# Kernel optimization log

Hardware: AMD Instinct MI355X
Metric: run time of the kernel (lower is better)

## Reference

```python
import jax, jax.numpy as jnp
import numpy as np

B, T = 64, 1024
RNN_DIM = 256          # lstm input/hidden dim
HID2 = 512             # 2*rnn_hidden_dim (bi-encoder output per char)
POS_DIM = 100
POS_SIZE = 48
LABEL = 96
POS_PAD = 0
APP_ID = 1


def setup_inputs() -> dict:
    key = jax.random.key(0)
    ks = jax.random.split(key, 9)
    s = 0.1
    enc = jax.random.normal(ks[0], (B, T, HID2), jnp.float32)
    pos_id = jax.random.randint(ks[1], (T, B), 0, POS_SIZE)
    start_index = jax.random.randint(ks[2], (T, B), 0, T)
    pos_table = (jax.random.normal(ks[3], (POS_SIZE, POS_DIM), jnp.float32) * s).at[POS_PAD].set(0.0)
    W_ih = jax.random.normal(ks[4], (4 * RNN_DIM, RNN_DIM), jnp.float32) * s
    b_ih = jnp.zeros((4 * RNN_DIM,), jnp.float32)
    W_hh = jax.random.normal(ks[5], (4 * RNN_DIM, RNN_DIM), jnp.float32) * s
    b_hh = jnp.zeros((4 * RNN_DIM,), jnp.float32)
    comb_W = jax.random.normal(ks[6], (RNN_DIM, HID2 + POS_DIM), jnp.float32) * s
    comb_b = jnp.zeros((RNN_DIM,), jnp.float32)
    lin_W = jax.random.normal(ks[7], (LABEL, HID2 + RNN_DIM), jnp.float32) * s
    return {"encoder_out": enc, "pos_table": pos_table, "W_ih": W_ih, "b_ih": b_ih,
            "W_hh": W_hh, "b_hh": b_hh, "comb_W": comb_W, "comb_b": comb_b,
            "lin_W": lin_W, "pos_id": pos_id, "start_index": start_index}


def reference(encoder_out, pos_table, W_ih, b_ih, W_hh, b_hh, comb_W, comb_b, lin_W,
              pos_id, start_index):
    Bn, Tn, D2 = encoder_out.shape
    H = W_hh.shape[1]
    L = lin_W.shape[0]
    dt = encoder_out.dtype
    # prefix sums: P[:, t] = sum of encoder_out[:, :t]  -> [B, T+1, D2]
    P = jnp.concatenate([jnp.zeros((Bn, 1, D2), dt), jnp.cumsum(encoder_out, axis=1)], axis=1)
    # step t consumes decisions made at step t-1 (state.pos_id[-1] / words_startindex[-1])
    prev_pos = jnp.concatenate([jnp.zeros((1, Bn), pos_id.dtype), pos_id[:-1]], axis=0)
    prev_start = jnp.concatenate([jnp.zeros((1, Bn), start_index.dtype), start_index[:-1]], axis=0)
    ts = jnp.arange(Tn)
    enc_t = jnp.swapaxes(encoder_out, 0, 1)   # [T, B, D2]
    P_t = jnp.swapaxes(P[:, :Tn], 0, 1)       # [T, B, D2]; P_t[t] = prefix up to t
    barange = jnp.arange(Bn)
    lab = jnp.arange(L)

    def step(carry, xs):
        h, c = carry
        t, pp, ps, Pt, et = xs
        # variable-length word avg-pool over chars [start, t)  (F.avg_pool1d)
        valid = (ps >= 0) & (t > 0)
        start = jnp.clip(jnp.minimum(ps, t - 1), 0, Tn - 1)
        wsum = Pt - P[barange, start]                       # [B, D2]
        length = jnp.maximum(t - start, 1).astype(dt)
        avg = jnp.where(valid[:, None], wsum / length[:, None], jnp.zeros((), dt))
        pe = pos_table[pp]                                  # [B, pos_dim]
        z = jnp.tanh(jnp.concatenate([pe, avg], axis=1) @ comb_W.T + comb_b)
        z = jnp.where(t > 0, z, jnp.zeros((), dt))          # t==0: z bucket of zeros
        # LSTMCell
        gates = z @ W_ih.T + b_ih + h @ W_hh.T + b_hh
        i_g, f_g, g_g, o_g = jnp.split(gates, 4, axis=1)
        c_new = jax.nn.sigmoid(f_g) * c + jax.nn.sigmoid(i_g) * jnp.tanh(g_g)
        h_new = jax.nn.sigmoid(o_g) * jnp.tanh(c_new)
        # output projection over [h_now, encoder_out[t]]
        out = jnp.concatenate([h_new, et], axis=1) @ lin_W.T
        out = jnp.where((t == 0) & (lab[None, :] == APP_ID), jnp.asarray(-1e10, dt), out)
        return (h_new, c_new), out

    h0 = jnp.zeros((Bn, H), dt)
    (_, _), outs = jax.lax.scan(step, (h0, h0), (ts, prev_pos, prev_start, P_t, enc_t))
    dec = jnp.swapaxes(outs, 0, 1).reshape(Bn * Tn, L)   # cat along dim 1 then view
    return jax.nn.log_softmax(dec, axis=1)
```

## Files before the change

### kernel.cpp

```cpp
#include <hip/hip_runtime.h>

typedef unsigned short u16;
typedef unsigned int u32;
typedef unsigned long long u64;
typedef __attribute__((ext_vector_type(8))) short short8;
typedef __attribute__((ext_vector_type(4))) float f32x4;
typedef __attribute__((ext_vector_type(4))) unsigned int u32x4;

#define B_ 64
#define T_ 1024
#define D2_ 512
#define HD_ 256
#define G4_ 1024
#define PD_ 100
#define KX_ 640
#define KO_ 768
#define LBL_ 96
#define LPAD_ 128

__device__ __forceinline__ float bf2f(u16 u) {
  u32 v = ((u32)u) << 16;
  return __builtin_bit_cast(float, v);
}
__device__ __forceinline__ u16 f2bf(float f) {
  u32 u = __builtin_bit_cast(u32, f);
  u32 r = (u + 0x7fffu + ((u >> 16) & 1u)) >> 16;
  return (u16)r;
}
__device__ __forceinline__ u32 pk2(float a, float b) {
  return (u32)f2bf(a) | ((u32)f2bf(b) << 16);
}
__device__ __forceinline__ float sgm(float x) {
  return __builtin_amdgcn_rcpf(1.f + __builtin_amdgcn_exp2f(-1.442695040888963f * x));
}
__device__ __forceinline__ float thh(float x) {
  return fmaf(-2.f,
              __builtin_amdgcn_rcpf(1.f + __builtin_amdgcn_exp2f(2.885390081777927f * x)),
              1.f);
}
__device__ __forceinline__ u32 enc4(float y) {
  float a = fabsf(y);
  u32 c = 0;
  c = a >= 0.25f ? 1u : c;
  c = a >= 0.75f ? 2u : c;
  c = a >= 1.25f ? 3u : c;
  c = a >= 1.75f ? 4u : c;
  c = a >= 2.5f ? 5u : c;
  c = a >= 3.5f ? 6u : c;
  c = a >= 5.0f ? 7u : c;
  return c | ((__builtin_bit_cast(u32, y) >> 28) & 8u);
}
__device__ __forceinline__ f32x4 mfma4_init(u32x4 a, u32x4 b, f32x4 c) {
  f32x4 d;
  asm volatile("v_mfma_f32_16x16x128_f8f6f4 %0, %1, %2, %3 cbsz:4 blgp:4"
               : "=&a"(d)
               : "v"(a), "a"(b), "a"(c));
  return d;
}
__device__ __forceinline__ void mfma4_acc(f32x4& d, u32x4 a, u32x4 b) {
  asm volatile("v_mfma_f32_16x16x128_f8f6f4 %0, %1, %2, %0 cbsz:4 blgp:4"
               : "+a"(d)
               : "v"(a), "a"(b));
}

__global__ __launch_bounds__(256) void k_prep(
    const float* combW, const float* Wih, const float* bih, const float* Whh,
    const float* bhh, const float* linW, u16* wc, u16* wih, u32* w4, u16* wlin,
    float* biasg) {
  int idx = blockIdx.x * 256 + threadIdx.x;
  if (idx < 256 * KX_) {
    int r = idx / KX_, c = idx % KX_;
    wc[idx] = f2bf(c < 612 ? combW[r * 612 + c] : 0.f);
    return;
  }
  idx -= 256 * KX_;
  if (idx < G4_ * HD_) { wih[idx] = f2bf(Wih[idx]); return; }
  idx -= G4_ * HD_;
  if (idx < G4_ * HD_ / 8) {
    int n = idx >> 5, c0 = (idx & 31) * 8;
    const float* wr = Whh + n * 256 + c0;
    u32 word = 0;
#pragma unroll
    for (int i = 0; i < 4; ++i) {
      u32 byte = enc4(wr[2 * i] * 8.f) | (enc4(wr[2 * i + 1] * 8.f) << 4);
      word |= byte << (8 * i);
    }
    w4[n * 32 + (c0 >> 3)] = word;
    return;
  }
  idx -= G4_ * HD_ / 8;
  if (idx < LPAD_ * KO_) {
    int r = idx / KO_;
    wlin[idx] = f2bf(r < LBL_ ? linW[idx] : 0.f);
    return;
  }
  idx -= LPAD_ * KO_;
  if (idx < G4_) biasg[idx] = bih[idx] + bhh[idx];
}

__global__ __launch_bounds__(512) void k_psum(const float* enc, float* S) {
  const int bc = blockIdx.x;
  const int d = threadIdx.x;
  const int b = bc >> 4, c = bc & 15;
  const float* e = enc + (((size_t)b * T_) + c * 64) * D2_ + d;
  float s = 0.f;
#pragma unroll 8
  for (int j = 0; j < 64; ++j) s += e[(size_t)j * D2_];
  S[(size_t)bc * D2_ + d] = s;
}

__global__ __launch_bounds__(512) void k_pwrite(const float* enc, const float* S,
                                                float* P) {
  const int bc = blockIdx.x;
  const int d = threadIdx.x;
  const int b = bc >> 4, c = bc & 15;
  float off = 0.f;
  for (int c2 = 0; c2 < c; ++c2) off += S[((size_t)(b * 16 + c2)) * D2_ + d];
  const float* e = enc + (((size_t)b * T_) + c * 64) * D2_ + d;
  float* p = P + (((size_t)b * T_) + c * 64) * D2_ + d;
#pragma unroll 4
  for (int j = 0; j < 64; ++j) {
    p[(size_t)j * D2_] = off;
    off += e[(size_t)j * D2_];
  }
}

__global__ __launch_bounds__(320) void k_xbuild(const float* P, const float* ptab,
                                                const int* pid, const int* sidx,
                                                u16* X) {
  const int tid = threadIdx.x;
  const int row = tid / 80;
  const int ir = tid - row * 80;
  const int m = blockIdx.x * 4 + row;
  const int t = m >> 6, b = m & 63;
  int pp = 0, ps = 0;
  if (t > 0) {
    pp = pid[(t - 1) * B_ + b];
    ps = sidx[(t - 1) * B_ + b];
  }
  bool valid = (ps >= 0) && (t > 0);
  int start = min(ps, t - 1);
  start = max(start, 0);
  start = min(start, T_ - 1);
  float invlen = 1.f / (float)max(t - start, 1);
  const float* Pt = P + ((size_t)b * T_ + t) * D2_;
  const float* Ps = P + ((size_t)b * T_ + start) * D2_;
  const int k0 = ir * 8;
  uint4 o;
  if (k0 >= 104 && k0 + 8 <= 612) {
    if (valid) {
      int d = k0 - 100;
      float4 t0 = *(const float4*)(Pt + d), t1 = *(const float4*)(Pt + d + 4);
      float4 s0 = *(const float4*)(Ps + d), s1 = *(const float4*)(Ps + d + 4);
      o.x = pk2((t0.x - s0.x) * invlen, (t0.y - s0.y) * invlen);
      o.y = pk2((t0.z - s0.z) * invlen, (t0.w - s0.w) * invlen);
      o.z = pk2((t1.x - s1.x) * invlen, (t1.y - s1.y) * invlen);
      o.w = pk2((t1.z - s1.z) * invlen, (t1.w - s1.w) * invlen);
    } else {
      o = (uint4){0, 0, 0, 0};
    }
  } else if (k0 + 8 <= 100) {
    const float* pr = ptab + pp * PD_ + k0;
    o.x = pk2(pr[0], pr[1]);
    o.y = pk2(pr[2], pr[3]);
    o.z = pk2(pr[4], pr[5]);
    o.w = pk2(pr[6], pr[7]);
  } else if (k0 >= 616) {
    o = (uint4){0, 0, 0, 0};
  } else {
    u32 ow[4];
#pragma unroll
    for (int j2 = 0; j2 < 4; ++j2) {
      float v[2];
#pragma unroll
      for (int jj = 0; jj < 2; ++jj) {
        int k = k0 + j2 * 2 + jj;
        float x;
        if (k < PD_) x = ptab[pp * PD_ + k];
        else if (k < 612) x = valid ? (Pt[k - PD_] - Ps[k - PD_]) * invlen : 0.f;
        else x = 0.f;
        v[jj] = x;
      }
      ow[j2] = pk2(v[0], v[1]);
    }
    o = (uint4){ow[0], ow[1], ow[2], ow[3]};
  }
  *(uint4*)(X + (size_t)m * KX_ + k0) = o;
}

template <int MODE>
__global__ __launch_bounds__(256, 2) void k_gemm(const u16* A, const u16* Bw,
                                                 const float* bias, u16* outb) {
  constexpr int K = (MODE == 0) ? KX_ : HD_;
  constexpr int NOUT = (MODE == 0) ? 256 : 1024;
  __shared__ u16 As[128][40];
  __shared__ u16 Bs[128][40];
  const int m0 = blockIdx.x * 128, n0 = blockIdx.y * 128;
  const int tid = threadIdx.x;
  const int w = tid >> 6, l = tid & 63;
  const int wr = w >> 1, wc = w & 1;
  const int l15 = l & 15, lh = l >> 4;
  const int srow = tid >> 2, sc8 = (tid & 3) * 8;
  int brow0, brow1;
  if constexpr (MODE == 1) {
    int j0 = n0 + srow, j1 = n0 + srow + 64;
    brow0 = (j0 & 3) * 256 + (j0 >> 2);
    brow1 = (j1 & 3) * 256 + (j1 >> 2);
  } else {
    brow0 = n0 + srow;
    brow1 = n0 + srow + 64;
  }
  f32x4 acc[4][4] = {};
  for (int k0 = 0; k0 < K; k0 += 32) {
    uint4 a0 = *(const uint4*)(A + (size_t)(m0 + srow) * K + k0 + sc8);
    uint4 a1 = *(const uint4*)(A + (size_t)(m0 + srow + 64) * K + k0 + sc8);
    uint4 b0 = *(const uint4*)(Bw + (size_t)brow0 * K + k0 + sc8);
    uint4 b1 = *(const uint4*)(Bw + (size_t)brow1 * K + k0 + sc8);
    __syncthreads();
    *(uint4*)&As[srow][sc8] = a0;
    *(uint4*)&As[srow + 64][sc8] = a1;
    *(uint4*)&Bs[srow][sc8] = b0;
    *(uint4*)&Bs[srow + 64][sc8] = b1;
    __syncthreads();
    short8 af[4], bf[4];
#pragma unroll
    for (int i = 0; i < 4; ++i) {
      af[i] = *(const short8*)&As[wr * 64 + i * 16 + l15][lh * 8];
      bf[i] = *(const short8*)&Bs[wc * 64 + i * 16 + l15][lh * 8];
    }
#pragma unroll
    for (int mi = 0; mi < 4; ++mi)
#pragma unroll
      for (int ni = 0; ni < 4; ++ni)
        acc[mi][ni] =
            __builtin_amdgcn_mfma_f32_16x16x32_bf16(af[mi], bf[ni], acc[mi][ni], 0, 0, 0);
  }
#pragma unroll
  for (int mi = 0; mi < 4; ++mi)
#pragma unroll
    for (int ni = 0; ni < 4; ++ni)
#pragma unroll
      for (int r = 0; r < 4; ++r) {
        int gm = m0 + wr * 64 + mi * 16 + lh * 4 + r;
        int gn = n0 + wc * 64 + ni * 16 + l15;
        float v = acc[mi][ni][r];
        if constexpr (MODE == 0) {
          v = tanhf(v + bias[gn]);
          if (gm < 64) v = 0.f;
          outb[(size_t)gm * NOUT + gn] = f2bf(v);
        } else {
          v += bias[(gn & 3) * 256 + (gn >> 2)];
          outb[(size_t)gm * NOUT + gn] = f2bf(v);
        }
      }
}

__global__ __launch_bounds__(512, 2) void k_seq(const u16* G, const u32* w4,
                                                u16* Hout) {
  __shared__ __align__(16) unsigned char hq[2][128];
  const int b = blockIdx.x;
  const int tid = threadIdx.x;
  const int w = tid >> 6, l = tid & 63;
  const int c16 = l & 15, quad = l >> 4;
  const unsigned char* w4b = (const unsigned char*)w4;
  u32x4 Bf[2][4][2];
#pragma unroll
  for (int ct = 0; ct < 2; ++ct)
#pragma unroll
    for (int g = 0; g < 4; ++g) {
      int n = g * 256 + w * 32 + ct * 16 + c16;
#pragma unroll
      for (int kb = 0; kb < 2; ++kb)
        Bf[ct][g][kb] =
            *(const u32x4*)(w4b + (size_t)n * 128 + kb * 64 + quad * 16);
    }
  f32x4 Z4 = (f32x4){0.f, 0.f, 0.f, 0.f};
  asm volatile("" : "+a"(Z4));
  if (tid < 128) hq[0][tid] = 0;
  const int myct = quad >> 1;
  const int mycell = w * 32 + myct * 16 + c16;
  const u16* gptr = G + (size_t)b * 1024 + mycell * 4;
  u64 gq = *(const u64*)gptr;
  float cc = 0.f;
  int cur = 0;
  __syncthreads();
  for (int t = 0; t < T_; ++t) {
    int tn = (t + 1 < T_) ? t + 1 : t;
    u64 ngq = *(const u64*)(gptr + (size_t)tn * 65536);
    u32x4 a0 = *(const u32x4*)&hq[cur][quad * 16];
    u32x4 a1 = *(const u32x4*)&hq[cur][64 + quad * 16];
    f32x4 acc[2][4];
#pragma unroll
    for (int ct = 0; ct < 2; ++ct)
#pragma unroll
      for (int g = 0; g < 4; ++g) acc[ct][g] = mfma4_init(a0, Bf[ct][g][0], Z4);
#pragma unroll
    for (int ct = 0; ct < 2; ++ct)
#pragma unroll
      for (int g = 0; g < 4; ++g) mfma4_acc(acc[ct][g], a1, Bf[ct][g][1]);
    __builtin_amdgcn_sched_barrier(0);
    asm volatile("s_nop 7\n\ts_nop 7\n\ts_nop 7");
    bool hi = (myct != 0);
    float vi = fmaf(hi ? acc[1][0][0] : acc[0][0][0], 0.03125f, bf2f((u16)gq));
    float vf = fmaf(hi ? acc[1][1][0] : acc[0][1][0], 0.03125f, bf2f((u16)(gq >> 16)));
    float vg = fmaf(hi ? acc[1][2][0] : acc[0][2][0], 0.03125f, bf2f((u16)(gq >> 32)));
    float vo = fmaf(hi ? acc[1][3][0] : acc[0][3][0], 0.03125f, bf2f((u16)(gq >> 48)));
    cc = sgm(vf) * cc + sgm(vi) * thh(vg);
    float h = sgm(vo) * thh(cc);
    u32 nib = enc4(h * 4.f);
    u32 nib2 = (u32)__shfl_xor((int)nib, 1);
    if ((quad & 1) == 0) {
      if ((c16 & 1) == 0)
        hq[cur ^ 1][mycell >> 1] = (unsigned char)(nib | (nib2 << 4));
      Hout[((size_t)b * 1024 + t) * 256 + mycell] = f2bf(h);
    }
    gq = ngq;
    cur ^= 1;
    __syncthreads();
  }
}

__global__ __launch_bounds__(256) void k_out(const u16* Hs, const float* enc,
                                             const u16* wlin, float* out) {
  __shared__ u16 As[64][40];
  __shared__ u16 Bs[128][40];
  const int m0 = blockIdx.x * 64;
  const int tid = threadIdx.x;
  const int srow = tid >> 2, sc8 = (tid & 3) * 8;
  const int brow = tid >> 1, bc16 = (tid & 1) * 16;
  const int w = tid >> 6, l = tid & 63;
  const int l15 = l & 15, lh = l >> 4;
  f32x4 acc[8] = {};
  for (int k0 = 0; k0 < KO_; k0 += 32) {
    int k = k0 + sc8;
    uint4 av;
    if (k < 256) {
      av = *(const uint4*)(Hs + (size_t)(m0 + srow) * 256 + k);
    } else {
      const float* src = enc + (size_t)(m0 + srow) * 512 + (k - 256);
      float4 f0 = *(const float4*)(src);
      float4 f1 = *(const float4*)(src + 4);
      av.x = pk2(f0.x, f0.y);
      av.y = pk2(f0.z, f0.w);
      av.z = pk2(f1.x, f1.y);
      av.w = pk2(f1.z, f1.w);
    }
    *(uint4*)&As[srow][sc8] = av;
    const u16* bsrc = wlin + (size_t)brow * KO_ + k0 + bc16;
    *(uint4*)&Bs[brow][bc16] = *(const uint4*)(bsrc);
    *(uint4*)&Bs[brow][bc16 + 8] = *(const uint4*)(bsrc + 8);
    __syncthreads();
    short8 a8 = *(const short8*)&As[16 * w + l15][lh * 8];
#pragma unroll
    for (int nt = 0; nt < 8; ++nt) {
      short8 b8 = *(const short8*)&Bs[nt * 16 + l15][lh * 8];
      acc[nt] = __builtin_amdgcn_mfma_f32_16x16x32_bf16(a8, b8, acc[nt], 0, 0, 0);
    }
    __syncthreads();
  }
#pragma unroll
  for (int r = 0; r < 4; ++r) {
    int gm = m0 + 16 * w + lh * 4 + r;
    float v[8];
#pragma unroll
    for (int nt = 0; nt < 8; ++nt) v[nt] = acc[nt][r];
    if ((gm & (T_ - 1)) == 0 && l15 == 1) v[0] = -1e10f;
    float mx = v[0];
#pragma unroll
    for (int nt = 1; nt < 6; ++nt) mx = fmaxf(mx, v[nt]);
#pragma unroll
    for (int s = 1; s < 16; s <<= 1) mx = fmaxf(mx, __shfl_xor(mx, s));
    float s0 = 0.f;
#pragma unroll
    for (int nt = 0; nt < 6; ++nt)
      s0 += __builtin_amdgcn_exp2f(1.442695040888963f * (v[nt] - mx));
#pragma unroll
    for (int s = 1; s < 16; s <<= 1) s0 += __shfl_xor(s0, s);
    float lg = __builtin_amdgcn_logf(s0) * 0.6931471805599453f + mx;
#pragma unroll
    for (int nt = 0; nt < 6; ++nt)
      out[(size_t)gm * LBL_ + nt * 16 + l15] = v[nt] - lg;
  }
}

extern "C" void kernel_launch(void* const* d_in, const int* in_sizes, int n_in,
                              void* d_out, int out_size, void* d_ws, size_t ws_size,
                              hipStream_t stream) {
  const float* enc = (const float*)d_in[0];
  const float* ptab = (const float*)d_in[1];
  const float* Wih = (const float*)d_in[2];
  const float* bih = (const float*)d_in[3];
  const float* Whh = (const float*)d_in[4];
  const float* bhh = (const float*)d_in[5];
  const float* combW = (const float*)d_in[6];
  const float* combb = (const float*)d_in[7];
  const float* linW = (const float*)d_in[8];
  const int* pid = (const int*)d_in[9];
  const int* sidx = (const int*)d_in[10];

  char* ws = (char*)d_ws;
  size_t off = 0;
  auto alloc = [&](size_t bytes) {
    void* p = ws + off;
    off += (bytes + 255) & ~(size_t)255;
    return p;
  };
  float* P = (float*)alloc((size_t)B_ * T_ * D2_ * 4);
  u16* Xb = (u16*)alloc((size_t)T_ * B_ * KX_ * 2);
  u16* Z = (u16*)alloc((size_t)T_ * B_ * HD_ * 2);
  u16* wc = (u16*)alloc(256 * KX_ * 2);
  u16* wih = (u16*)alloc(G4_ * HD_ * 2);
  u32* w4 = (u32*)alloc(G4_ * HD_ / 2);
  u16* wlin = (u16*)alloc(LPAD_ * KO_ * 2);
  float* biasg = (float*)alloc(G4_ * 4);
  u16* G = (u16*)P;
  u16* Hs = (u16*)Xb;
  float* S = (float*)Z;
  float* out = (float*)d_out;

  k_prep<<<2180, 256, 0, stream>>>(combW, Wih, bih, Whh, bhh, linW, wc, wih, w4,
                                   wlin, biasg);
  k_psum<<<B_ * 16, 512, 0, stream>>>(enc, S);
  k_pwrite<<<B_ * 16, 512, 0, stream>>>(enc, S, P);
  k_xbuild<<<T_ * B_ / 4, 320, 0, stream>>>(P, ptab, pid, sidx, Xb);
  dim3 g3(512, 2);
  k_gemm<0><<<g3, 256, 0, stream>>>(Xb, wc, combb, Z);
  dim3 g4(512, 8);
  k_gemm<1><<<g4, 256, 0, stream>>>(Z, wih, biasg, G);
  k_seq<<<B_, 512, 0, stream>>>(G, w4, Hs);
  k_out<<<1024, 256, 0, stream>>>(Hs, enc, wlin, out);
}
```

Before: 944.2 us.

## Split LSTM recurrence over 16 waves, one column tile per wave

The sequential LSTM kernel now launches 1024 threads (16 waves) per batch element instead of 512. Each wave owns a single 16-column tile per gate, so it issues half as many MFMAs per step and holds half the weight fragments. The goal is a shorter critical path per timestep, at the cost of a block-wide barrier spanning twice as many waves and only one quad of each wave storing results.

```diff
diff --git a/kernel.cpp b/kernel.cpp
--- a/kernel.cpp
+++ b/kernel.cpp
@@ -255,30 +255,26 @@
       }
 }
 
-__global__ __launch_bounds__(512, 2) void k_seq(const u16* G, const u32* w4,
-                                                u16* Hout) {
+__global__ __launch_bounds__(1024, 4) void k_seq(const u16* G, const u32* w4,
+                                                 u16* Hout) {
   __shared__ __align__(16) unsigned char hq[2][128];
   const int b = blockIdx.x;
   const int tid = threadIdx.x;
   const int w = tid >> 6, l = tid & 63;
   const int c16 = l & 15, quad = l >> 4;
   const unsigned char* w4b = (const unsigned char*)w4;
-  u32x4 Bf[2][4][2];
-#pragma unroll
-  for (int ct = 0; ct < 2; ++ct)
-#pragma unroll
-    for (int g = 0; g < 4; ++g) {
-      int n = g * 256 + w * 32 + ct * 16 + c16;
-#pragma unroll
-      for (int kb = 0; kb < 2; ++kb)
-        Bf[ct][g][kb] =
-            *(const u32x4*)(w4b + (size_t)n * 128 + kb * 64 + quad * 16);
-    }
+  const int mycell = w * 16 + c16;
+  u32x4 Bf[4][2];
+#pragma unroll
+  for (int g = 0; g < 4; ++g) {
+    int n = g * 256 + mycell;
+#pragma unroll
+    for (int kb = 0; kb < 2; ++kb)
+      Bf[g][kb] = *(const u32x4*)(w4b + (size_t)n * 128 + kb * 64 + quad * 16);
+  }
   f32x4 Z4 = (f32x4){0.f, 0.f, 0.f, 0.f};
   asm volatile("" : "+a"(Z4));
   if (tid < 128) hq[0][tid] = 0;
-  const int myct = quad >> 1;
-  const int mycell = w * 32 + myct * 16 + c16;
   const u16* gptr = G + (size_t)b * 1024 + mycell * 4;
   u64 gq = *(const u64*)gptr;
   float cc = 0.f;
@@ -289,27 +285,22 @@
     u64 ngq = *(const u64*)(gptr + (size_t)tn * 65536);
     u32x4 a0 = *(const u32x4*)&hq[cur][quad * 16];
     u32x4 a1 = *(const u32x4*)&hq[cur][64 + quad * 16];
-    f32x4 acc[2][4];
-#pragma unroll
-    for (int ct = 0; ct < 2; ++ct)
-#pragma unroll
-      for (int g = 0; g < 4; ++g) acc[ct][g] = mfma4_init(a0, Bf[ct][g][0], Z4);
-#pragma unroll
-    for (int ct = 0; ct < 2; ++ct)
-#pragma unroll
-      for (int g = 0; g < 4; ++g) mfma4_acc(acc[ct][g], a1, Bf[ct][g][1]);
+    f32x4 acc[4];
+#pragma unroll
+    for (int g = 0; g < 4; ++g) acc[g] = mfma4_init(a0, Bf[g][0], Z4);
+#pragma unroll
+    for (int g = 0; g < 4; ++g) mfma4_acc(acc[g], a1, Bf[g][1]);
     __builtin_amdgcn_sched_barrier(0);
     asm volatile("s_nop 7\n\ts_nop 7\n\ts_nop 7");
-    bool hi = (myct != 0);
-    float vi = fmaf(hi ? acc[1][0][0] : acc[0][0][0], 0.03125f, bf2f((u16)gq));
-    float vf = fmaf(hi ? acc[1][1][0] : acc[0][1][0], 0.03125f, bf2f((u16)(gq >> 16)));
-    float vg = fmaf(hi ? acc[1][2][0] : acc[0][2][0], 0.03125f, bf2f((u16)(gq >> 32)));
-    float vo = fmaf(hi ? acc[1][3][0] : acc[0][3][0], 0.03125f, bf2f((u16)(gq >> 48)));
+    float vi = fmaf(acc[0][0], 0.03125f, bf2f((u16)gq));
+    float vf = fmaf(acc[1][0], 0.03125f, bf2f((u16)(gq >> 16)));
+    float vg = fmaf(acc[2][0], 0.03125f, bf2f((u16)(gq >> 32)));
+    float vo = fmaf(acc[3][0], 0.03125f, bf2f((u16)(gq >> 48)));
     cc = sgm(vf) * cc + sgm(vi) * thh(vg);
     float h = sgm(vo) * thh(cc);
     u32 nib = enc4(h * 4.f);
     u32 nib2 = (u32)__shfl_xor((int)nib, 1);
-    if ((quad & 1) == 0) {
+    if (quad == 0) {
       if ((c16 & 1) == 0)
         hq[cur ^ 1][mycell >> 1] = (unsigned char)(nib | (nib2 << 4));
       Hout[((size_t)b * 1024 + t) * 256 + mycell] = f2bf(h);
@@ -427,6 +418,6 @@
   k_gemm<0><<<g3, 256, 0, stream>>>(Xb, wc, combb, Z);
   dim3 g4(512, 8);
   k_gemm<1><<<g4, 256, 0, stream>>>(Z, wih, biasg, G);
-  k_seq<<<B_, 512, 0, stream>>>(G, w4, Hs);
+  k_seq<<<B_, 1024, 0, stream>>>(G, w4, Hs);
   k_out<<<1024, 256, 0, stream>>>(Hs, enc, wlin, out);
 }
```

New measurement: 1.097 ms. 1.16x slower.
